# Optimization experiments

Measured on AMD Instinct MI355X. Metric: run time of the kernel, lower is better.

The kernel has to match this reference:

```python
import jax, jax.numpy as jnp
import numpy as np
from jax.ops import segment_sum

N_NODES = 100000
N_EDGES = 3200000
NUM_FEATURES = 256


def setup_inputs() -> dict:
    key = jax.random.key(0)
    ks = jax.random.split(key, 12)
    def lin(k, fan_in, fan_out):
        bound = 1.0 / np.sqrt(fan_in)
        kw, kb = jax.random.split(k)
        W = jax.random.uniform(kw, (fan_in, fan_out), jnp.float32, -bound, bound)
        b = jax.random.uniform(kb, (fan_out,), jnp.float32, -bound, bound)
        return W, b
    x = jax.random.normal(ks[0], (N_NODES, NUM_FEATURES), jnp.float32)
    edge_index = jax.random.randint(ks[1], (2, N_EDGES), 0, N_NODES, jnp.int64 if jax.config.jax_enable_x64 else jnp.int32)
    W1, b1 = lin(ks[2], NUM_FEATURES, 64)
    W2, b2 = lin(ks[3], 64, 32)
    W3, b3 = lin(ks[4], 32, 16)
    Ws02, bs02 = lin(ks[5], NUM_FEATURES, 32)
    Ws03, bs03 = lin(ks[6], NUM_FEATURES, 16)
    Ws13, bs13 = lin(ks[7], 64, 16)
    Wout, bout = lin(ks[8], 16, 1)
    return dict(x=x, edge_index=edge_index, W1=W1, b1=b1, W2=W2, b2=b2,
                W3=W3, b3=b3, Ws02=Ws02, bs02=bs02, Ws03=Ws03, bs03=bs03,
                Ws13=Ws13, bs13=bs13, Wout=Wout, bout=bout)


def _deg_inv_sqrt(edge_index, n_nodes):
    # gcn_norm with self-loops: degree counted at target nodes, +1 for self-loop
    dst = edge_index[1]
    deg = segment_sum(jnp.ones(edge_index.shape[1], jnp.float32), dst, num_segments=n_nodes) + 1.0
    return jnp.where(deg > 0, jax.lax.rsqrt(deg), 0.0)


def _gcn_conv(x, W, b, edge_index, dinv):
    # PyG GCNConv: h = x W; out[i] = sum_{j->i} dinv[j]*dinv[i]*h[j] + dinv[i]^2*h[i] + b
    src, dst = edge_index[0], edge_index[1]
    h = x @ W                                   # [N, out]
    norm = (dinv[src] * dinv[dst])[:, None]     # [E, 1]
    agg = segment_sum(h[src] * norm, dst, num_segments=x.shape[0])
    agg = agg + (dinv * dinv)[:, None] * h      # self-loop term
    return agg + b


def reference(x, edge_index, W1, b1, W2, b2, W3, b3,
              Ws02, bs02, Ws03, bs03, Ws13, bs13, Wout, bout):
    # Dropout in eval mode (identity).
    dinv = _deg_inv_sqrt(edge_index, x.shape[0])
    x1 = jax.nn.relu(_gcn_conv(x, W1, b1, edge_index, dinv))
    x2 = jax.nn.relu(_gcn_conv(x1, W2, b2, edge_index, dinv) + x @ Ws02 + bs02)
    x3 = jax.nn.relu(_gcn_conv(x2, W3, b3, edge_index, dinv)
                     + x @ Ws03 + bs03 + x1 @ Ws13 + bs13)
    return jax.nn.sigmoid(x3 @ Wout + bout)
```

## Files before the change

### kernel.cpp

```cpp
#include <hip/hip_runtime.h>
#include <hip/hip_bf16.h>
#include <math.h>


#define NBUCK_MAX 512
#define P1_CHUNK 4096
#define EPT 16
#define BCAP 9216
#define PREP_BLOCKS 142
#define HIST_BLOCKS 1024

typedef __attribute__((ext_vector_type(8))) short bfrag;
typedef __attribute__((ext_vector_type(4))) float f4_t;
typedef __attribute__((ext_vector_type(2))) float f2_t;

__device__ inline float uaf(unsigned u) { return __uint_as_float(u); }
__device__ inline ushort f2bf(float f) {
    __hip_bfloat16 b = __float2bfloat16(f);
    return *reinterpret_cast<ushort*>(&b);
}
__device__ inline bfrag cvt8(const float4 a, const float4 b) {
    union { ushort u[8]; bfrag f; } r;
    r.u[0] = f2bf(a.x); r.u[1] = f2bf(a.y); r.u[2] = f2bf(a.z); r.u[3] = f2bf(a.w);
    r.u[4] = f2bf(b.x); r.u[5] = f2bf(b.y); r.u[6] = f2bf(b.z); r.u[7] = f2bf(b.w);
    return r.f;
}
__device__ inline bfrag ld_bfrag(const ushort* p) {
    const uint4 raw = *reinterpret_cast<const uint4*>(p);
    return *reinterpret_cast<const bfrag*>(&raw);
}


__global__ __launch_bounds__(256) void fka_kernel(
    const float* __restrict__ W1, const float* __restrict__ Ws02,
    const float* __restrict__ Ws03, const float* __restrict__ W2,
    const float* __restrict__ Ws13, const float* __restrict__ W3,
    ushort* __restrict__ Wt0, ushort* __restrict__ Wt1, ushort* __restrict__ Wt2,
    const int* __restrict__ dst, int E, int* __restrict__ bucket_count,
    int nbuckets)
{
    if (blockIdx.x < PREP_BLOCKS) {
        const int idx = blockIdx.x * 256 + threadIdx.x;
        if (idx < 32768) {
            int f = idx >> 8, k = idx & 255;
            float v = 0.f;
            if (f < 64)       v = W1[k * 64 + f];
            else if (f < 96)  v = Ws02[k * 32 + (f - 64)];
            else if (f < 112) v = Ws03[k * 16 + (f - 96)];
            Wt0[idx] = f2bf(v);
        } else if (idx < 32768 + 3072) {
            int t = idx - 32768;
            int f = t >> 6, k = t & 63;
            float v = (f < 32) ? W2[k * 32 + f] : Ws13[k * 16 + (f - 32)];
            Wt1[t] = f2bf(v);
        } else if (idx < 32768 + 3072 + 512) {
            int t = idx - 32768 - 3072;
            int f = t >> 5, k = t & 31;
            Wt2[t] = f2bf(W3[k * 16 + f]);
        }
        return;
    }
    __shared__ int lhist[NBUCK_MAX];
    const int bid = blockIdx.x - PREP_BLOCKS;
    for (int i = threadIdx.x; i < nbuckets; i += 256) lhist[i] = 0;
    __syncthreads();
    const int stride = HIST_BLOCKS * 256;
    for (int e = bid * 256 + threadIdx.x; e < E; e += stride)
        atomicAdd(&lhist[dst[e] >> 8], 1);
    __syncthreads();
    for (int i = threadIdx.x; i < nbuckets; i += 256) {
        int c = lhist[i];
        if (c) atomicAdd(&bucket_count[i], c);
    }
}


__global__ __launch_bounds__(512) void bucket_scan_kernel(
    const int* __restrict__ bucket_count, int* __restrict__ bucket_base,
    int* __restrict__ bucket_cursor, int nbuckets)
{
    __shared__ int tmp[512];
    const int tid = threadIdx.x;
    int v = (tid < nbuckets) ? bucket_count[tid] : 0;
    tmp[tid] = v;
    __syncthreads();
    for (int off = 1; off < 512; off <<= 1) {
        int t = (tid >= off) ? tmp[tid - off] : 0;
        __syncthreads();
        tmp[tid] += t;
        __syncthreads();
    }
    if (tid < nbuckets) {
        int base = tmp[tid] - v;
        bucket_base[tid]   = base;
        bucket_cursor[tid] = base;
    }
}


union FKBsh {
    float xs[2][4096];
    struct {
        int hist[NBUCK_MAX];
        int lofs[NBUCK_MAX];
        int gbase[NBUCK_MAX];
        int lcur[NBUCK_MAX];
        int ssum[256];
        unsigned int stage[P1_CHUNK];
        int gidx[P1_CHUNK];
    } p;
};

__global__ __launch_bounds__(256, 3) void fkb_kernel(
    const int* __restrict__ src, const int* __restrict__ dst, int E,
    int* __restrict__ bucket_cursor, unsigned int* __restrict__ keys,
    int nbuckets, int part_blocks,
    const float* __restrict__ X, const ushort* __restrict__ Wt0,
    const float* __restrict__ bs02, const float* __restrict__ bs03,
    ushort* __restrict__ g1, float* __restrict__ pre2,
    float* __restrict__ pre3, int N)
{
    __shared__ __align__(16) FKBsh sh;
    const int tid = threadIdx.x;

    if (blockIdx.x < part_blocks) {
        const int e0 = blockIdx.x * P1_CHUNK;
        const int nE = min(P1_CHUNK, E - e0);

        for (int i = tid; i < NBUCK_MAX; i += 256) { sh.p.hist[i] = 0; sh.p.lcur[i] = 0; }
        __syncthreads();

        int myb[EPT];
        unsigned int mypk[EPT];
#pragma unroll
        for (int j = 0; j < EPT; ++j) {
            const int e = e0 + tid + j * 256;
            if (e < E) {
                const int d = dst[e];
                myb[j]  = d >> 8;
                mypk[j] = ((unsigned int)(d & 255) << 17) | (unsigned int)src[e];
                atomicAdd(&sh.p.hist[myb[j]], 1);
            } else myb[j] = -1;
        }
        __syncthreads();

        int a0 = (2 * tid     < nbuckets) ? sh.p.hist[2 * tid]     : 0;
        int a1 = (2 * tid + 1 < nbuckets) ? sh.p.hist[2 * tid + 1] : 0;
        sh.p.ssum[tid] = a0 + a1;
        __syncthreads();
        for (int off = 1; off < 256; off <<= 1) {
            int t = (tid >= off) ? sh.p.ssum[tid - off] : 0;
            __syncthreads();
            sh.p.ssum[tid] += t;
            __syncthreads();
        }
        const int ex = sh.p.ssum[tid] - (a0 + a1);
        if (2 * tid     < nbuckets) sh.p.lofs[2 * tid]     = ex;
        if (2 * tid + 1 < nbuckets) sh.p.lofs[2 * tid + 1] = ex + a0;
        __syncthreads();

        for (int i = tid; i < nbuckets; i += 256)
            sh.p.gbase[i] = atomicAdd(&bucket_cursor[i], sh.p.hist[i]);
        __syncthreads();

#pragma unroll
        for (int j = 0; j < EPT; ++j) {
            if (myb[j] >= 0) {
                const int b = myb[j];
                const int l = sh.p.lofs[b] + atomicAdd(&sh.p.lcur[b], 1);
                sh.p.stage[l] = mypk[j];
                sh.p.gidx[l]  = sh.p.gbase[b] - sh.p.lofs[b] + l;
            }
        }
        __syncthreads();

        for (int i = tid; i < nE; i += 256)
            keys[sh.p.gidx[i]] = sh.p.stage[i];
        return;
    }

    const int bid  = blockIdx.x - part_blocks;
    const int lane = tid & 63;
    const int wf   = tid >> 6;
    const int n0   = bid * 64;
    const int mrow = lane & 15;
    const int q    = lane >> 4;
    const int kq   = q * 8;

    bfrag bfr[2][8];
#pragma unroll
    for (int ft = 0; ft < 2; ++ft) {
        const ushort* wr = &Wt0[(size_t)(wf * 32 + ft * 16 + mrow) * 256 + kq];
#pragma unroll
        for (int p = 0; p < 8; ++p)
            bfr[ft][p] = ld_bfrag(&wr[p * 32]);
    }

    int srow[4], schunk[4];
#pragma unroll
    for (int j = 0; j < 4; ++j) {
        const int R = wf * 16 + j * 4 + q;
        srow[j]   = min(n0 + R, N - 1);
        schunk[j] = mrow ^ (R & 7);
    }

    auto STAGE = [&](int buf, int kc) {
#pragma unroll
        for (int j = 0; j < 4; ++j) {
            const float* gsrc =
                X + (size_t)srow[j] * 256 + kc * 64 + schunk[j] * 4;
            __builtin_amdgcn_global_load_lds(
                (const __attribute__((address_space(1))) unsigned int*)gsrc,
                (__attribute__((address_space(3))) unsigned int*)
                    &sh.xs[buf][(wf * 16 + j * 4) * 64],
                16, 0, 0);
        }
    };

    f4_t acc[4][2];
#pragma unroll
    for (int a = 0; a < 4; ++a)
#pragma unroll
        for (int b = 0; b < 2; ++b) acc[a][b] = {0.f, 0.f, 0.f, 0.f};

    STAGE(0, 0);
    __syncthreads();

    int cur = 0;
    for (int kc = 0; kc < 4; ++kc) {
        if (kc < 3) STAGE(cur ^ 1, kc + 1);
        const float4* Xs4 = reinterpret_cast<const float4*>(&sh.xs[cur][0]);
#pragma unroll
        for (int pl = 0; pl < 2; ++pl) {
            bfrag af[4];
#pragma unroll
            for (int mt = 0; mt < 4; ++mt) {
                const int r  = mt * 16 + mrow;
                const int c0 = pl * 8 + q * 2;
                const float4 u0 = Xs4[r * 16 + (c0 ^ (r & 7))];
                const float4 u1 = Xs4[r * 16 + ((c0 + 1) ^ (r & 7))];
                af[mt] = cvt8(u0, u1);
            }
            const int pg = kc * 2 + pl;
#pragma unroll
            for (int mt = 0; mt < 4; ++mt)
#pragma unroll
                for (int ft = 0; ft < 2; ++ft)
                    acc[mt][ft] = __builtin_amdgcn_mfma_f32_16x16x32_bf16(
                        af[mt], bfr[ft][pg], acc[mt][ft], 0, 0, 0);
        }
        __syncthreads();
        cur ^= 1;
    }

    char* sm = (char*)&sh;
    ushort* g1s = (ushort*)sm;
    float*  p2s = (float*)(sm + 8192);
    float*  p3s = (float*)(sm + 16384);

    if (wf < 2) {
#pragma unroll
        for (int mt = 0; mt < 4; ++mt) {
#pragma unroll
            for (int r = 0; r < 4; ++r) {
                const int nl = mt * 16 + q * 4 + r;
#pragma unroll
                for (int ft = 0; ft < 2; ++ft)
                    g1s[nl * 64 + wf * 32 + ft * 16 + mrow] =
                        f2bf(acc[mt][ft][r]);
            }
        }
    } else if (wf == 2) {
#pragma unroll
        for (int mt = 0; mt < 4; ++mt)
#pragma unroll
            for (int ft = 0; ft < 2; ++ft)
#pragma unroll
                for (int r = 0; r < 4; ++r)
                    p2s[(mt * 16 + q * 4 + r) * 32 + ft * 16 + mrow] =
                        acc[mt][ft][r] + bs02[ft * 16 + mrow];
    } else {
#pragma unroll
        for (int mt = 0; mt < 4; ++mt)
#pragma unroll
            for (int r = 0; r < 4; ++r)
                p3s[(mt * 16 + q * 4 + r) * 16 + mrow] =
                    acc[mt][0][r] + bs03[mrow];
    }
    __syncthreads();

    const uint4* g1v = (const uint4*)g1s;
    const uint4* p2v = (const uint4*)p2s;
    const uint4* p3v = (const uint4*)p3s;
#pragma unroll
    for (int t = 0; t < 2; ++t) {
        const int i   = t * 256 + tid;
        const int row = i >> 3;
        if (n0 + row < N)
            *(uint4*)(g1 + (size_t)(n0 + row) * 64 + (i & 7) * 8) = g1v[i];
    }
#pragma unroll
    for (int t = 0; t < 2; ++t) {
        const int i   = t * 256 + tid;
        const int row = i >> 3;
        if (n0 + row < N)
            *(uint4*)(pre2 + (size_t)(n0 + row) * 32 + (i & 7) * 4) = p2v[i];
    }
    {
        const int i   = tid;
        const int row = i >> 2;
        if (n0 + row < N)
            *(uint4*)(pre3 + (size_t)(n0 + row) * 16 + (i & 3) * 4) = p3v[i];
    }
}


__global__ __launch_bounds__(256) void csr_build_kernel(
    const unsigned int* __restrict__ keys, const int* __restrict__ bucket_base,
    const int* __restrict__ bucket_count,
    int* __restrict__ row_off, float* __restrict__ dinv, int* __restrict__ col,
    int N, int E)
{
    __shared__ unsigned int inb[BCAP];
    __shared__ int outv[BCAP];
    __shared__ int hist[256];
    __shared__ int lofs[256];
    __shared__ int ssum[256];

    const int tid  = threadIdx.x;
    const int b    = blockIdx.x;
    const int base = bucket_base[b];
    const int cnt  = min(bucket_count[b], BCAP);
    const int n0   = b << 8;
    const int nn   = min(256, N - n0);

    for (int i = tid; i < cnt; i += 256) inb[i] = keys[base + i];
    hist[tid] = 0;
    __syncthreads();

    for (int i = tid; i < cnt; i += 256)
        atomicAdd(&hist[inb[i] >> 17], 1);
    __syncthreads();

    ssum[tid] = hist[tid];
    __syncthreads();
    for (int off = 1; off < 256; off <<= 1) {
        int t = (tid >= off) ? ssum[tid - off] : 0;
        __syncthreads();
        ssum[tid] += t;
        __syncthreads();
    }
    lofs[tid] = ssum[tid] - hist[tid];

    if (tid < nn) {
        row_off[n0 + tid] = base + lofs[tid];
        dinv[n0 + tid]    = rsqrtf((float)hist[tid] + 1.0f);
    }
    if (b == 0 && tid == 0) row_off[N] = E;
    __syncthreads();

    hist[tid] = 0;
    __syncthreads();

    for (int i = tid; i < cnt; i += 256) {
        const unsigned int k = inb[i];
        const int node = k >> 17;
        const int l = lofs[node] + atomicAdd(&hist[node], 1);
        outv[l] = (int)(k & 0x1FFFF);
    }
    __syncthreads();

    for (int i = tid; i < cnt; i += 256)
        col[base + i] = outv[i];
}


template<int F, int MODE>
__global__ __launch_bounds__(256) void agg_kernel(
    const ushort* __restrict__ g, const float* __restrict__ dinv,
    const int* __restrict__ row_off, const int* __restrict__ col,
    const float* __restrict__ bias, const float* __restrict__ pre,
    const ushort* __restrict__ Wk, const float* __restrict__ bs13,
    const float* __restrict__ Wout, const float* __restrict__ bout,
    void* __restrict__ out, float* __restrict__ pre3, int N)
{
    constexpr int FG  = F / 8;
    constexpr int EPW = 64 / FG;
    constexpr int U   = 32 / EPW;
    constexpr int LSH = (F == 64) ? 7 : (F == 32 ? 6 : 5);
    constexpr bool GDV = (MODE == 0);

    const int lane = threadIdx.x & 63;
    const int wv   = threadIdx.x >> 6;
    const int i    = blockIdx.x * 4 + wv;
    if (i >= N) return;

    const int fg  = lane & (FG - 1);
    const int eo  = lane / FG;
    const unsigned fbb = (unsigned)fg * 16;

    const char* gb = (const char*)g;

    f2_t acc0 = {0.f, 0.f}, acc1 = {0.f, 0.f};
    f2_t acc2 = {0.f, 0.f}, acc3 = {0.f, 0.f};

    const int s = row_off[i], e = row_off[i + 1];
    const int nfull = (e - s) >> 5;
    int p = s;
    const int* cp = col + s + eo;

    for (int it = 0; it < nfull; ++it, p += 32, cp += 32) {
        unsigned voff[U];
        float dv[U];
#pragma unroll
        for (int u = 0; u < U; ++u) {
            const int js = cp[u * EPW];
            voff[u] = ((unsigned)js << LSH) + fbb;
            if (GDV) dv[u] = dinv[js];
        }
        uint4 w[U];
#pragma unroll
        for (int u = 0; u < U; ++u)
            w[u] = *reinterpret_cast<const uint4*>(gb + voff[u]);
#pragma unroll
        for (int u = 0; u < U; ++u) {
            if (GDV) {
                const f2_t mm = {dv[u], dv[u]};
                acc0 += mm * (f2_t){uaf(w[u].x << 16), uaf(w[u].x & 0xffff0000u)};
                acc1 += mm * (f2_t){uaf(w[u].y << 16), uaf(w[u].y & 0xffff0000u)};
                acc2 += mm * (f2_t){uaf(w[u].z << 16), uaf(w[u].z & 0xffff0000u)};
                acc3 += mm * (f2_t){uaf(w[u].w << 16), uaf(w[u].w & 0xffff0000u)};
            } else {
                acc0 += (f2_t){uaf(w[u].x << 16), uaf(w[u].x & 0xffff0000u)};
                acc1 += (f2_t){uaf(w[u].y << 16), uaf(w[u].y & 0xffff0000u)};
                acc2 += (f2_t){uaf(w[u].z << 16), uaf(w[u].z & 0xffff0000u)};
                acc3 += (f2_t){uaf(w[u].w << 16), uaf(w[u].w & 0xffff0000u)};
            }
        }
    }
    if (p < e) {
        float m[U];
        unsigned voff[U];
#pragma unroll
        for (int u = 0; u < U; ++u) {
            const int q = p + eo + u * EPW;
            const int js = col[min(q, e - 1)];
            const float live = (q < e) ? 1.0f : 0.0f;
            m[u]    = GDV ? live * dinv[js] : live;
            voff[u] = ((unsigned)js << LSH) + fbb;
        }
        uint4 w[U];
#pragma unroll
        for (int u = 0; u < U; ++u)
            w[u] = *reinterpret_cast<const uint4*>(gb + voff[u]);
#pragma unroll
        for (int u = 0; u < U; ++u) {
            const f2_t mm = {m[u], m[u]};
            acc0 += mm * (f2_t){uaf(w[u].x << 16), uaf(w[u].x & 0xffff0000u)};
            acc1 += mm * (f2_t){uaf(w[u].y << 16), uaf(w[u].y & 0xffff0000u)};
            acc2 += mm * (f2_t){uaf(w[u].z << 16), uaf(w[u].z & 0xffff0000u)};
            acc3 += mm * (f2_t){uaf(w[u].w << 16), uaf(w[u].w & 0xffff0000u)};
        }
    }

#pragma unroll
    for (int ro = FG; ro < 64; ro <<= 1) {
        acc0.x += __shfl_xor(acc0.x, ro); acc0.y += __shfl_xor(acc0.y, ro);
        acc1.x += __shfl_xor(acc1.x, ro); acc1.y += __shfl_xor(acc1.y, ro);
        acc2.x += __shfl_xor(acc2.x, ro); acc2.y += __shfl_xor(acc2.y, ro);
        acc3.x += __shfl_xor(acc3.x, ro); acc3.y += __shfl_xor(acc3.y, ro);
    }

    const uint4 ws =
        *reinterpret_cast<const uint4*>(gb + (((unsigned)i) << LSH) + fbb);
    const float di = dinv[i];
    const float sw = GDV ? di * di : di;
    const int fb = fg * 8;
    const float4 b0 = *reinterpret_cast<const float4*>(&bias[fb]);
    const float4 b1 = *reinterpret_cast<const float4*>(&bias[fb + 4]);

    float v0 = di * acc0.x + sw * uaf(ws.x << 16)         + b0.x;
    float v1 = di * acc0.y + sw * uaf(ws.x & 0xffff0000u) + b0.y;
    float v2 = di * acc1.x + sw * uaf(ws.y << 16)         + b0.z;
    float v3 = di * acc1.y + sw * uaf(ws.y & 0xffff0000u) + b0.w;
    float v4 = di * acc2.x + sw * uaf(ws.z << 16)         + b1.x;
    float v5 = di * acc2.y + sw * uaf(ws.z & 0xffff0000u) + b1.y;
    float v6 = di * acc3.x + sw * uaf(ws.w << 16)         + b1.z;
    float v7 = di * acc3.y + sw * uaf(ws.w & 0xffff0000u) + b1.w;

    if (MODE != 0) {
        const float4 p0 = *reinterpret_cast<const float4*>(&pre[(size_t)i * F + fb]);
        const float4 p1 = *reinterpret_cast<const float4*>(&pre[(size_t)i * F + fb + 4]);
        v0 += p0.x; v1 += p0.y; v2 += p0.z; v3 += p0.w;
        v4 += p1.x; v5 += p1.y; v6 += p1.z; v7 += p1.w;
    }
    v0 = fmaxf(v0, 0.f); v1 = fmaxf(v1, 0.f);
    v2 = fmaxf(v2, 0.f); v3 = fmaxf(v3, 0.f);
    v4 = fmaxf(v4, 0.f); v5 = fmaxf(v5, 0.f);
    v6 = fmaxf(v6, 0.f); v7 = fmaxf(v7, 0.f);

    if (MODE == 0) {
        float pacc[6];
#pragma unroll
        for (int t = 0; t < 6; ++t) {
            const int f = eo * 6 + t;
            const uint4 wr = *reinterpret_cast<const uint4*>(&Wk[f * 64 + fb]);
            float sacc;
            sacc  = v0 * uaf(wr.x << 16);
            sacc += v1 * uaf(wr.x & 0xffff0000u);
            sacc += v2 * uaf(wr.y << 16);
            sacc += v3 * uaf(wr.y & 0xffff0000u);
            sacc += v4 * uaf(wr.z << 16);
            sacc += v5 * uaf(wr.z & 0xffff0000u);
            sacc += v6 * uaf(wr.w << 16);
            sacc += v7 * uaf(wr.w & 0xffff0000u);
            pacc[t] = sacc;
        }
#pragma unroll
        for (int t = 0; t < 6; ++t) {
            pacc[t] += __shfl_xor(pacc[t], 1);
            pacc[t] += __shfl_xor(pacc[t], 2);
            pacc[t] += __shfl_xor(pacc[t], 4);
        }
        if ((lane & 7) == 0) {
#pragma unroll
            for (int t = 0; t < 6; ++t) {
                const int f = eo * 6 + t;
                if (f < 32) {
                    ((ushort*)out)[(size_t)i * 32 + f] = f2bf(di * pacc[t]);
                } else {
                    pre3[(size_t)i * 16 + (f - 32)] += pacc[t] + bs13[f - 32];
                }
            }
        }
    } else if (MODE == 1) {
        const uint4 wr = *reinterpret_cast<const uint4*>(&Wk[eo * 32 + fb]);
        float sacc;
        sacc  = v0 * uaf(wr.x << 16);
        sacc += v1 * uaf(wr.x & 0xffff0000u);
        sacc += v2 * uaf(wr.y << 16);
        sacc += v3 * uaf(wr.y & 0xffff0000u);
        sacc += v4 * uaf(wr.z << 16);
        sacc += v5 * uaf(wr.z & 0xffff0000u);
        sacc += v6 * uaf(wr.w << 16);
        sacc += v7 * uaf(wr.w & 0xffff0000u);
        sacc += __shfl_xor(sacc, 1);
        sacc += __shfl_xor(sacc, 2);
        if ((lane & 3) == 0)
            ((ushort*)out)[(size_t)i * 16 + eo] = f2bf(di * sacc);
    } else {
        const float4 w0 = *reinterpret_cast<const float4*>(&Wout[fb]);
        const float4 w1 = *reinterpret_cast<const float4*>(&Wout[fb + 4]);
        float t = v0 * w0.x + v1 * w0.y + v2 * w0.z + v3 * w0.w +
                  v4 * w1.x + v5 * w1.y + v6 * w1.z + v7 * w1.w;
        t += __shfl_xor(t, 1);
        if (lane == 0)
            ((float*)out)[i] = 1.0f / (1.0f + expf(-(t + bout[0])));
    }
}


extern "C" void kernel_launch(void* const* d_in, const int* in_sizes, int n_in,
                              void* d_out, int out_size, void* d_ws, size_t ws_size,
                              hipStream_t stream)
{
    const float* x    = (const float*)d_in[0];
    const int*   edge = (const int*)d_in[1];
    const float* W1   = (const float*)d_in[2];
    const float* b1   = (const float*)d_in[3];
    const float* W2   = (const float*)d_in[4];
    const float* b2   = (const float*)d_in[5];
    const float* W3   = (const float*)d_in[6];
    const float* b3   = (const float*)d_in[7];
    const float* Ws02 = (const float*)d_in[8];
    const float* bs02 = (const float*)d_in[9];
    const float* Ws03 = (const float*)d_in[10];
    const float* bs03 = (const float*)d_in[11];
    const float* Ws13 = (const float*)d_in[12];
    const float* bs13 = (const float*)d_in[13];
    const float* Wout = (const float*)d_in[14];
    const float* bout = (const float*)d_in[15];

    const int N = in_sizes[0] / 256;
    const int E = in_sizes[1] / 2;
    const int* srcv = edge;
    const int* dstv = edge + E;
    const int nbuckets = (N + 255) >> 8;

    char* ws = (char*)d_ws;
    size_t off = 0;
    auto alloc = [&](size_t bytes) -> void* {
        void* p = ws + off;
        off += (bytes + 255) & ~(size_t)255;
        return p;
    };
    unsigned int* keys = (unsigned int*)alloc((size_t)E * 4);
    int*   col      = (int*)  alloc((size_t)E * 4);
    int*   bcount   = (int*)  alloc((size_t)NBUCK_MAX * 4);
    int*   bbase    = (int*)  alloc((size_t)NBUCK_MAX * 4);
    int*   bcursor  = (int*)  alloc((size_t)NBUCK_MAX * 4);
    int*   row_off  = (int*)  alloc((size_t)(N + 1) * 4);
    float* dinv     = (float*)alloc((size_t)N * 4);
    ushort* Wt0     = (ushort*)alloc((size_t)128 * 256 * 2);
    ushort* Wt1     = (ushort*)alloc((size_t)48 * 64 * 2);
    ushort* Wt2     = (ushort*)alloc((size_t)16 * 32 * 2);
    ushort* g1      = (ushort*)alloc((size_t)N * 64 * 2);
    ushort* g2      = (ushort*)alloc((size_t)N * 32 * 2);
    ushort* g3      = (ushort*)alloc((size_t)N * 16 * 2);
    float* pre2     = (float*)alloc((size_t)N * 32 * 4);
    float* pre3     = (float*)alloc((size_t)N * 16 * 4);

    hipMemsetAsync(bcount, 0, (size_t)NBUCK_MAX * 4, stream);

    fka_kernel<<<PREP_BLOCKS + HIST_BLOCKS, 256, 0, stream>>>(
        W1, Ws02, Ws03, W2, Ws13, W3, Wt0, Wt1, Wt2,
        dstv, E, bcount, nbuckets);

    bucket_scan_kernel<<<1, 512, 0, stream>>>(bcount, bbase, bcursor, nbuckets);

    const int PB = (E + P1_CHUNK - 1) / P1_CHUNK;
    fkb_kernel<<<PB + (N + 63) / 64, 256, 0, stream>>>(
        srcv, dstv, E, bcursor, keys, nbuckets, PB,
        x, Wt0, bs02, bs03, g1, pre2, pre3, N);

    csr_build_kernel<<<nbuckets, 256, 0, stream>>>(
        keys, bbase, bcount, row_off, dinv, col, N, E);

    const int ab = (N + 3) / 4;

    agg_kernel<64, 0><<<ab, 256, 0, stream>>>(
        g1, dinv, row_off, col, b1, nullptr, Wt1, bs13,
        nullptr, nullptr, g2, pre3, N);
    agg_kernel<32, 1><<<ab, 256, 0, stream>>>(
        g2, dinv, row_off, col, b2, pre2, Wt2, nullptr,
        nullptr, nullptr, g3, nullptr, N);
    agg_kernel<16, 2><<<ab, 256, 0, stream>>>(
        g3, dinv, row_off, col, b3, pre3, nullptr, nullptr,
        Wout, bout, d_out, nullptr, N);
}
```

Baseline: 454.1 us.

## Prescale g1 by dinv in CSR build and split layer-1 epilogue into MFMA GEMM

The layer-1 features g1 are now scaled by the source node's dinv inside the CSR build kernel. This removes the per-edge dinv gather in the first aggregation. The per-node 64x48 projection, previously done with scalar FMAs and shuffles in the agg epilogue, moves to a separate MFMA kernel that reads a new bf16 x1 buffer and writes g2 and the pre3 accumulation. This adds an extra kernel launch, an extra round trip of N*64 bf16 values through memory, and a second bf16 rounding of g1 after scaling.

```diff
diff --git a/kernel.cpp b/kernel.cpp
--- a/kernel.cpp
+++ b/kernel.cpp
@@ -18,6 +18,11 @@
 __device__ inline ushort f2bf(float f) {
     __hip_bfloat16 b = __float2bfloat16(f);
     return *reinterpret_cast<ushort*>(&b);
+}
+__device__ inline unsigned scale2(unsigned w, float s) {
+    const float lo = uaf(w << 16) * s;
+    const float hi = uaf(w & 0xffff0000u) * s;
+    return (unsigned)f2bf(lo) | ((unsigned)f2bf(hi) << 16);
 }
 __device__ inline bfrag cvt8(const float4 a, const float4 b) {
     union { ushort u[8]; bfrag f; } r;
@@ -319,13 +324,14 @@
     const unsigned int* __restrict__ keys, const int* __restrict__ bucket_base,
     const int* __restrict__ bucket_count,
     int* __restrict__ row_off, float* __restrict__ dinv, int* __restrict__ col,
-    int N, int E)
+    ushort* __restrict__ g1, int N, int E)
 {
     __shared__ unsigned int inb[BCAP];
     __shared__ int outv[BCAP];
     __shared__ int hist[256];
     __shared__ int lofs[256];
     __shared__ int ssum[256];
+    __shared__ float sdinv[256];
 
     const int tid  = threadIdx.x;
     const int b    = blockIdx.x;
@@ -353,11 +359,23 @@
     lofs[tid] = ssum[tid] - hist[tid];
 
     if (tid < nn) {
+        const float dv = rsqrtf((float)hist[tid] + 1.0f);
         row_off[n0 + tid] = base + lofs[tid];
-        dinv[n0 + tid]    = rsqrtf((float)hist[tid] + 1.0f);
+        dinv[n0 + tid]    = dv;
+        sdinv[tid]        = dv;
     }
     if (b == 0 && tid == 0) row_off[N] = E;
     __syncthreads();
+
+    for (int i = tid; i < nn * 8; i += 256) {
+        const int row = i >> 3, ch = i & 7;
+        uint4* pp = reinterpret_cast<uint4*>(g1 + (size_t)(n0 + row) * 64 + ch * 8);
+        const float dv = sdinv[row];
+        uint4 v = *pp;
+        v.x = scale2(v.x, dv); v.y = scale2(v.y, dv);
+        v.z = scale2(v.z, dv); v.w = scale2(v.w, dv);
+        *pp = v;
+    }
 
     hist[tid] = 0;
     __syncthreads();
@@ -375,20 +393,108 @@
 }
 
 
+__global__ __launch_bounds__(256) void gemm_mfma1(
+    const ushort* __restrict__ X1, const ushort* __restrict__ Wt1,
+    const float* __restrict__ bs13, const float* __restrict__ dinv,
+    __hip_bfloat16* __restrict__ g2, float* __restrict__ pre3, int N)
+{
+    __shared__ __align__(16) ushort g2s[128 * 32];
+    __shared__ __align__(16) float  p3s[128 * 16];
+
+    const int tid  = threadIdx.x;
+    const int lane = tid & 63;
+    const int wave = tid >> 6;
+    const int nb   = blockIdx.x * 128;
+    const int n0   = nb + wave * 32;
+    const int mrow = lane & 15;
+    const int q    = lane >> 4;
+    const int kq   = q * 8;
+
+    f4_t acc[2][3];
+#pragma unroll
+    for (int a = 0; a < 2; ++a)
+#pragma unroll
+        for (int b = 0; b < 3; ++b) acc[a][b] = {0.f, 0.f, 0.f, 0.f};
+
+    const ushort* xrow[2];
+#pragma unroll
+    for (int mt = 0; mt < 2; ++mt) {
+        int r = n0 + mt * 16 + mrow;
+        r = (r < N) ? r : (N - 1);
+        xrow[mt] = &X1[(size_t)r * 64 + kq];
+    }
+    const ushort* wrow[3];
+#pragma unroll
+    for (int ft = 0; ft < 3; ++ft)
+        wrow[ft] = &Wt1[(size_t)(ft * 16 + mrow) * 64 + kq];
+
+#pragma unroll
+    for (int p = 0; p < 2; ++p) {
+        bfrag af[2], bf[3];
+#pragma unroll
+        for (int mt = 0; mt < 2; ++mt) af[mt] = ld_bfrag(&xrow[mt][p * 32]);
+#pragma unroll
+        for (int ft = 0; ft < 3; ++ft) bf[ft] = ld_bfrag(&wrow[ft][p * 32]);
+#pragma unroll
+        for (int mt = 0; mt < 2; ++mt)
+#pragma unroll
+            for (int ft = 0; ft < 3; ++ft)
+                acc[mt][ft] = __builtin_amdgcn_mfma_f32_16x16x32_bf16(
+                    af[mt], bf[ft], acc[mt][ft], 0, 0, 0);
+    }
+
+#pragma unroll
+    for (int mt = 0; mt < 2; ++mt) {
+#pragma unroll
+        for (int r = 0; r < 4; ++r) {
+            const int nl = wave * 32 + mt * 16 + q * 4 + r;
+            const float di = dinv[min(nb + nl, N - 1)];
+            g2s[nl * 32 +      mrow] = f2bf(di * acc[mt][0][r]);
+            g2s[nl * 32 + 16 + mrow] = f2bf(di * acc[mt][1][r]);
+            p3s[nl * 16 + mrow] = acc[mt][2][r] + bs13[mrow];
+        }
+    }
+    __syncthreads();
+
+    const uint4*  g2v = (const uint4*)g2s;
+    const float4* p3v = (const float4*)p3s;
+#pragma unroll
+    for (int t = 0; t < 2; ++t) {
+        const int i   = t * 256 + tid;
+        const int row = i >> 2;
+        if (nb + row < N)
+            *(uint4*)((ushort*)g2 + (size_t)(nb + row) * 32 + (i & 3) * 8) =
+                g2v[i];
+    }
+#pragma unroll
+    for (int t = 0; t < 2; ++t) {
+        const int i   = t * 256 + tid;
+        const int row = i >> 2;
+        if (nb + row < N) {
+            float4* dst =
+                (float4*)(pre3 + (size_t)(nb + row) * 16 + (i & 3) * 4);
+            float4 v = *dst;
+            const float4 s = p3v[i];
+            v.x += s.x; v.y += s.y; v.z += s.z; v.w += s.w;
+            *dst = v;
+        }
+    }
+}
+
+
 template<int F, int MODE>
 __global__ __launch_bounds__(256) void agg_kernel(
     const ushort* __restrict__ g, const float* __restrict__ dinv,
     const int* __restrict__ row_off, const int* __restrict__ col,
     const float* __restrict__ bias, const float* __restrict__ pre,
-    const ushort* __restrict__ Wk, const float* __restrict__ bs13,
+    const ushort* __restrict__ Wk,
     const float* __restrict__ Wout, const float* __restrict__ bout,
-    void* __restrict__ out, float* __restrict__ pre3, int N)
+    void* __restrict__ out, int N)
 {
     constexpr int FG  = F / 8;
     constexpr int EPW = 64 / FG;
     constexpr int U   = 32 / EPW;
     constexpr int LSH = (F == 64) ? 7 : (F == 32 ? 6 : 5);
-    constexpr bool GDV = (MODE == 0);
 
     const int lane = threadIdx.x & 63;
     const int wv   = threadIdx.x >> 6;
@@ -411,31 +517,19 @@
 
     for (int it = 0; it < nfull; ++it, p += 32, cp += 32) {
         unsigned voff[U];
-        float dv[U];
-#pragma unroll
-        for (int u = 0; u < U; ++u) {
-            const int js = cp[u * EPW];
-            voff[u] = ((unsigned)js << LSH) + fbb;
-            if (GDV) dv[u] = dinv[js];
-        }
+#pragma unroll
+        for (int u = 0; u < U; ++u)
+            voff[u] = ((unsigned)cp[u * EPW] << LSH) + fbb;
         uint4 w[U];
 #pragma unroll
         for (int u = 0; u < U; ++u)
             w[u] = *reinterpret_cast<const uint4*>(gb + voff[u]);
 #pragma unroll
         for (int u = 0; u < U; ++u) {
-            if (GDV) {
-                const f2_t mm = {dv[u], dv[u]};
-                acc0 += mm * (f2_t){uaf(w[u].x << 16), uaf(w[u].x & 0xffff0000u)};
-                acc1 += mm * (f2_t){uaf(w[u].y << 16), uaf(w[u].y & 0xffff0000u)};
-                acc2 += mm * (f2_t){uaf(w[u].z << 16), uaf(w[u].z & 0xffff0000u)};
-                acc3 += mm * (f2_t){uaf(w[u].w << 16), uaf(w[u].w & 0xffff0000u)};
-            } else {
-                acc0 += (f2_t){uaf(w[u].x << 16), uaf(w[u].x & 0xffff0000u)};
-                acc1 += (f2_t){uaf(w[u].y << 16), uaf(w[u].y & 0xffff0000u)};
-                acc2 += (f2_t){uaf(w[u].z << 16), uaf(w[u].z & 0xffff0000u)};
-                acc3 += (f2_t){uaf(w[u].w << 16), uaf(w[u].w & 0xffff0000u)};
-            }
+            acc0 += (f2_t){uaf(w[u].x << 16), uaf(w[u].x & 0xffff0000u)};
+            acc1 += (f2_t){uaf(w[u].y << 16), uaf(w[u].y & 0xffff0000u)};
+            acc2 += (f2_t){uaf(w[u].z << 16), uaf(w[u].z & 0xffff0000u)};
+            acc3 += (f2_t){uaf(w[u].w << 16), uaf(w[u].w & 0xffff0000u)};
         }
     }
     if (p < e) {
@@ -444,10 +538,8 @@
 #pragma unroll
         for (int u = 0; u < U; ++u) {
             const int q = p + eo + u * EPW;
-            const int js = col[min(q, e - 1)];
-            const float live = (q < e) ? 1.0f : 0.0f;
-            m[u]    = GDV ? live * dinv[js] : live;
-            voff[u] = ((unsigned)js << LSH) + fbb;
+            m[u]    = (q < e) ? 1.0f : 0.0f;
+            voff[u] = ((unsigned)col[min(q, e - 1)] << LSH) + fbb;
         }
         uint4 w[U];
 #pragma unroll
@@ -474,19 +566,18 @@
     const uint4 ws =
         *reinterpret_cast<const uint4*>(gb + (((unsigned)i) << LSH) + fbb);
     const float di = dinv[i];
-    const float sw = GDV ? di * di : di;
     const int fb = fg * 8;
     const float4 b0 = *reinterpret_cast<const float4*>(&bias[fb]);
     const float4 b1 = *reinterpret_cast<const float4*>(&bias[fb + 4]);
 
-    float v0 = di * acc0.x + sw * uaf(ws.x << 16)         + b0.x;
-    float v1 = di * acc0.y + sw * uaf(ws.x & 0xffff0000u) + b0.y;
-    float v2 = di * acc1.x + sw * uaf(ws.y << 16)         + b0.z;
-    float v3 = di * acc1.y + sw * uaf(ws.y & 0xffff0000u) + b0.w;
-    float v4 = di * acc2.x + sw * uaf(ws.z << 16)         + b1.x;
-    float v5 = di * acc2.y + sw * uaf(ws.z & 0xffff0000u) + b1.y;
-    float v6 = di * acc3.x + sw * uaf(ws.w << 16)         + b1.z;
-    float v7 = di * acc3.y + sw * uaf(ws.w & 0xffff0000u) + b1.w;
+    float v0 = di * (acc0.x + uaf(ws.x << 16))         + b0.x;
+    float v1 = di * (acc0.y + uaf(ws.x & 0xffff0000u)) + b0.y;
+    float v2 = di * (acc1.x + uaf(ws.y << 16))         + b0.z;
+    float v3 = di * (acc1.y + uaf(ws.y & 0xffff0000u)) + b0.w;
+    float v4 = di * (acc2.x + uaf(ws.z << 16))         + b1.x;
+    float v5 = di * (acc2.y + uaf(ws.z & 0xffff0000u)) + b1.y;
+    float v6 = di * (acc3.x + uaf(ws.w << 16))         + b1.z;
+    float v7 = di * (acc3.y + uaf(ws.w & 0xffff0000u)) + b1.w;
 
     if (MODE != 0) {
         const float4 p0 = *reinterpret_cast<const float4*>(&pre[(size_t)i * F + fb]);
@@ -500,38 +591,13 @@
     v6 = fmaxf(v6, 0.f); v7 = fmaxf(v7, 0.f);
 
     if (MODE == 0) {
-        float pacc[6];
-#pragma unroll
-        for (int t = 0; t < 6; ++t) {
-            const int f = eo * 6 + t;
-            const uint4 wr = *reinterpret_cast<const uint4*>(&Wk[f * 64 + fb]);
-            float sacc;
-            sacc  = v0 * uaf(wr.x << 16);
-            sacc += v1 * uaf(wr.x & 0xffff0000u);
-            sacc += v2 * uaf(wr.y << 16);
-            sacc += v3 * uaf(wr.y & 0xffff0000u);
-            sacc += v4 * uaf(wr.z << 16);
-            sacc += v5 * uaf(wr.z & 0xffff0000u);
-            sacc += v6 * uaf(wr.w << 16);
-            sacc += v7 * uaf(wr.w & 0xffff0000u);
-            pacc[t] = sacc;
-        }
-#pragma unroll
-        for (int t = 0; t < 6; ++t) {
-            pacc[t] += __shfl_xor(pacc[t], 1);
-            pacc[t] += __shfl_xor(pacc[t], 2);
-            pacc[t] += __shfl_xor(pacc[t], 4);
-        }
-        if ((lane & 7) == 0) {
-#pragma unroll
-            for (int t = 0; t < 6; ++t) {
-                const int f = eo * 6 + t;
-                if (f < 32) {
-                    ((ushort*)out)[(size_t)i * 32 + f] = f2bf(di * pacc[t]);
-                } else {
-                    pre3[(size_t)i * 16 + (f - 32)] += pacc[t] + bs13[f - 32];
-                }
-            }
+        if (lane < FG) {
+            uint4 o;
+            o.x = (unsigned)f2bf(v0) | ((unsigned)f2bf(v1) << 16);
+            o.y = (unsigned)f2bf(v2) | ((unsigned)f2bf(v3) << 16);
+            o.z = (unsigned)f2bf(v4) | ((unsigned)f2bf(v5) << 16);
+            o.w = (unsigned)f2bf(v6) | ((unsigned)f2bf(v7) << 16);
+            *reinterpret_cast<uint4*>((char*)out + (((size_t)i) << LSH) + fbb) = o;
         }
     } else if (MODE == 1) {
         const uint4 wr = *reinterpret_cast<const uint4*>(&Wk[eo * 32 + fb]);
@@ -605,6 +671,7 @@
     ushort* Wt1     = (ushort*)alloc((size_t)48 * 64 * 2);
     ushort* Wt2     = (ushort*)alloc((size_t)16 * 32 * 2);
     ushort* g1      = (ushort*)alloc((size_t)N * 64 * 2);
+    ushort* x1      = (ushort*)alloc((size_t)N * 64 * 2);
     ushort* g2      = (ushort*)alloc((size_t)N * 32 * 2);
     ushort* g3      = (ushort*)alloc((size_t)N * 16 * 2);
     float* pre2     = (float*)alloc((size_t)N * 32 * 4);
@@ -624,17 +691,19 @@
         x, Wt0, bs02, bs03, g1, pre2, pre3, N);
 
     csr_build_kernel<<<nbuckets, 256, 0, stream>>>(
-        keys, bbase, bcount, row_off, dinv, col, N, E);
+        keys, bbase, bcount, row_off, dinv, col, g1, N, E);
 
     const int ab = (N + 3) / 4;
 
     agg_kernel<64, 0><<<ab, 256, 0, stream>>>(
-        g1, dinv, row_off, col, b1, nullptr, Wt1, bs13,
-        nullptr, nullptr, g2, pre3, N);
+        g1, dinv, row_off, col, b1, nullptr, nullptr,
+        nullptr, nullptr, x1, N);
+    gemm_mfma1<<<(N + 127) / 128, 256, 0, stream>>>(
+        x1, Wt1, bs13, dinv, (__hip_bfloat16*)g2, pre3, N);
     agg_kernel<32, 1><<<ab, 256, 0, stream>>>(
-        g2, dinv, row_off, col, b2, pre2, Wt2, nullptr,
-        nullptr, nullptr, g3, nullptr, N);
+        g2, dinv, row_off, col, b2, pre2, Wt2,
+        nullptr, nullptr, g3, N);
     agg_kernel<16, 2><<<ab, 256, 0, stream>>>(
-        g3, dinv, row_off, col, b3, pre3, nullptr, nullptr,
-        Wout, bout, d_out, nullptr, N);
-}
+        g3, dinv, row_off, col, b3, pre3, nullptr,
+        Wout, bout, d_out, N);
+}
```

New measurement: 426.5 us. 1.06x faster.
